# Performance work log

Measured on AMD Instinct MI355X. Metric: run time of the kernel, lower is better.

## Reference

```python
import jax, jax.numpy as jnp
import numpy as np

N_A, N_D = 16384, 16384
D_EV = 4096      # d_inEvents (= rows of H_M)
H_DIM = 512      # hidden_dim
H1 = 1024        # hidden_dim1
H3 = 1024        # hidden_dim3
D_M = 4096       # d_inM (reconstruction output dim)


def _mlp2(x, w1, b1, w2, b2):
    return jax.nn.relu(x @ w1 + b1) @ w2 + b2


def setup_inputs() -> dict:
    key = jax.random.key(0)
    ks = jax.random.split(key, 32)
    s_in = (2.0 / D_EV) ** 0.5
    s_h1 = (2.0 / H1) ** 0.5
    s_2h = (2.0 / (2 * H_DIM)) ** 0.5
    s_h3 = (2.0 / H3) ** 0.5
    d = {
        "H_A": jax.random.uniform(ks[0], (N_A, D_EV), jnp.float32),
        "H_D": jax.random.uniform(ks[1], (N_D, D_EV), jnp.float32),
        "H_M": jax.random.uniform(ks[2], (D_EV, D_EV), jnp.float32),
    }
    for i, nm in enumerate(["A", "D", "M"]):
        d[f"w{nm}1"] = jax.random.normal(ks[3 + 4 * i], (D_EV, H1), jnp.float32) * s_in
        d[f"b{nm}1"] = jnp.zeros((H1,), jnp.float32)
        d[f"w{nm}2"] = jax.random.normal(ks[4 + 4 * i], (H1, H_DIM), jnp.float32) * s_h1
        d[f"b{nm}2"] = jnp.zeros((H_DIM,), jnp.float32)
    for i, nm in enumerate(["EA", "ED"]):
        d[f"w{nm}1"] = jax.random.normal(ks[16 + 4 * i], (2 * H_DIM, H3), jnp.float32) * s_2h
        d[f"b{nm}1"] = jnp.zeros((H3,), jnp.float32)
        d[f"w{nm}2"] = jax.random.normal(ks[17 + 4 * i], (H3, D_M), jnp.float32) * s_h3
        d[f"b{nm}2"] = jnp.zeros((D_M,), jnp.float32)
    return d


def reference(H_A, H_D, H_M,
              wA1, bA1, wA2, bA2,
              wD1, bD1, wD2, bD2,
              wM1, bM1, wM2, bM2,
              wEA1, bEA1, wEA2, bEA2,
              wED1, bED1, wED2, bED2):
    # Encoder (the torch.eye matmul is an identity and is elided)
    H_mean_A = _mlp2(H_A, wA1, bA1, wA2, bA2)   # [N_A, H_DIM]
    H_mean_D = _mlp2(H_D, wD1, bD1, wD2, bD2)   # [N_D, H_DIM]
    H_mean_M = _mlp2(H_M, wM1, bM1, wM2, bM2)   # [D_EV, H_DIM]
    # Pooling: per-column loop in torch == single matmul H^T @ H_mean
    sum_A = H_A.T @ H_mean_A                    # [D_EV, H_DIM]
    sum_D = H_D.T @ H_mean_D                    # [D_EV, H_DIM]
    EventA = jnp.concatenate([H_mean_M, sum_A], axis=1)  # [D_EV, 2*H_DIM]
    EventD = jnp.concatenate([H_mean_M, sum_D], axis=1)
    reconstructA = _mlp2(EventA, wEA1, bEA1, wEA2, bEA2)  # [D_EV, D_M]
    reconstructD = _mlp2(EventD, wED1, bED1, wED2, bED2)
    return (reconstructA, reconstructD, H_mean_A, H_mean_D, H_mean_M)
```

## Files before the change

kernel.cpp:

```cpp
#include <hip/hip_runtime.h>
#include <cstdint>
#include <cstddef>


typedef unsigned short u16;
typedef unsigned int u32;
typedef __bf16 bf16_t;
typedef bf16_t bf16x8 __attribute__((ext_vector_type(8)));
typedef float f32x4 __attribute__((ext_vector_type(4)));
typedef u16 u16x4 __attribute__((ext_vector_type(4)));
typedef u16 u16x8 __attribute__((ext_vector_type(8)));

__device__ __forceinline__ u16 f2bf(float x) {
  u32 u = __builtin_bit_cast(u32, x);
  u += 0x7FFFu + ((u >> 16) & 1u);
  return (u16)(u >> 16);
}
__device__ __forceinline__ float bf2f(u16 h) {
  u32 u = ((u32)h) << 16;
  return __builtin_bit_cast(float, u);
}

#define AS1(p) ((__attribute__((address_space(1))) void*)(p))
#define AS3(p) ((__attribute__((address_space(3))) void*)(p))

__global__ void detect_kernel(const u32* __restrict__ p, int* __restrict__ flag) {
  if (threadIdx.x == 0 && blockIdx.x == 0) {
    int cnt = 0;
    for (int i = 0; i < 64; ++i) {
      u32 b = (p[i] >> 8) & 0xFFu;
      cnt += (b >= 0x3Au && b < 0x40u) ? 1 : 0;
    }
    *flag = (cnt >= 32) ? 1 : 0;
  }
}

__global__ void convert_kernel(const void* __restrict__ src, u16* __restrict__ dst,
                               long n, const int* __restrict__ fl) {
  long i = ((long)blockIdx.x * 256 + threadIdx.x) * 8;
  if (i >= n) return;
  u16x8 r;
  if (*fl) {
    r = *(const u16x8*)((const u16*)src + i);
  } else {
    const float* s = (const float*)src + i;
#pragma unroll
    for (int j = 0; j < 8; ++j) r[j] = f2bf(s[j]);
  }
  *(u16x8*)(dst + i) = r;
}

__global__ void tconv_kernel(const void* __restrict__ src, long soff, u16* __restrict__ dst,
                             int R, int C, const int* __restrict__ fl) {
  __shared__ u16 t[32][33];
  const int dt = *fl;
  const int tx = threadIdx.x & 31, ty = threadIdx.x >> 5;
  const long c0 = (long)blockIdx.x * 32, r0 = (long)blockIdx.y * 32;
#pragma unroll
  for (int r = 0; r < 4; ++r) {
    int rr = ty * 4 + r;
    long off = soff + (r0 + rr) * (long)C + c0 + tx;
    t[rr][tx] = dt ? ((const u16*)src)[off] : f2bf(((const float*)src)[off]);
  }
  __syncthreads();
#pragma unroll
  for (int r = 0; r < 4; ++r) {
    int rr = ty * 4 + r;
    dst[(c0 + rr) * (long)R + r0 + tx] = t[tx][rr];
  }
}

__global__ void reduce4_kernel(const float* __restrict__ s, long stride,
                               u16* __restrict__ dst, long ldd, long n, int cl,
                               const void* __restrict__ bias, int relu,
                               const int* __restrict__ fl) {
  long i = (long)blockIdx.x * 256 + threadIdx.x;
  if (i >= n) return;
  float v = s[i] + s[i + stride] + s[i + 2 * stride] + s[i + 3 * stride];
  long col = i & ((1L << cl) - 1);
  if (bias) v += (*fl) ? bf2f(((const u16*)bias)[col]) : ((const float*)bias)[col];
  if (relu) v = v > 0.f ? v : 0.f;
  dst[(i >> cl) * ldd + col] = f2bf(v);
}

__global__ __launch_bounds__(256) void gemm_bt_kernel(
    const u16* __restrict__ A, long lda,
    const u16* __restrict__ Bt, long ldb,
    long K,
    const void* __restrict__ bias, int relu,
    void* __restrict__ outd, long odoff, long ldod,
    float* __restrict__ outw, long ldow, long ozstride,
    u16* __restrict__ outb, long ldob,
    u16* __restrict__ outb2, long ldob2,
    u16* __restrict__ outT, long ldT,
    const int* __restrict__ fl) {
  __shared__ u16 As[128 * 32];
  __shared__ u16 Bs[128 * 32];

  const int t = threadIdx.x;
  const int l = t & 63;
  const int w = t >> 6;
  const int wx = w & 1, wy = w >> 1;
  const long m0 = (long)blockIdx.y * 128;
  const long n0 = (long)blockIdx.x * 128;
  const int dt = *fl;

  const long koff = (long)blockIdx.z * K;
  A += koff;
  Bt += koff;
  if (outw) outw += (long)blockIdx.z * ozstride;

  const int srow = w * 16 + (l >> 2);
  const int scol = (((l & 3) ^ ((l >> 2) & 3))) * 8;
  const int la = l & 15, lq = l >> 4;
  const int fsl = (lq ^ (la & 3)) * 8;

  f32x4 acc[4][4];
  const f32x4 zero = {0.f, 0.f, 0.f, 0.f};
#pragma unroll
  for (int i = 0; i < 4; ++i)
#pragma unroll
    for (int j = 0; j < 4; ++j) acc[i][j] = zero;

  for (long k0 = 0; k0 < K; k0 += 32) {
#pragma unroll
    for (int r = 0; r < 2; ++r) {
      const u16* ga = A + (m0 + r * 64 + srow) * lda + k0 + scol;
      __builtin_amdgcn_global_load_lds(AS1(ga), AS3(As + (r * 64 + w * 16) * 32), 16, 0, 0);
      const u16* gb = Bt + (n0 + r * 64 + srow) * ldb + k0 + scol;
      __builtin_amdgcn_global_load_lds(AS1(gb), AS3(Bs + (r * 64 + w * 16) * 32), 16, 0, 0);
    }
    __syncthreads();

    bf16x8 af[4], bfr[4];
#pragma unroll
    for (int i = 0; i < 4; ++i) {
      af[i] = *(const bf16x8*)(As + (wy * 64 + i * 16 + la) * 32 + fsl);
      bfr[i] = *(const bf16x8*)(Bs + (wx * 64 + i * 16 + la) * 32 + fsl);
    }
#pragma unroll
    for (int i = 0; i < 4; ++i)
#pragma unroll
      for (int j = 0; j < 4; ++j)
        acc[i][j] = __builtin_amdgcn_mfma_f32_16x16x32_bf16(af[i], bfr[j], acc[i][j], 0, 0, 0);
    __syncthreads();
  }

  const long gr0 = m0 + wy * 64;
  const long gc0 = n0 + wx * 64;
#pragma unroll
  for (int i = 0; i < 4; ++i) {
#pragma unroll
    for (int j = 0; j < 4; ++j) {
      const long gc = gc0 + j * 16 + la;
      const long grb = gr0 + i * 16 + lq * 4;
      float bv = 0.f;
      if (bias) bv = dt ? bf2f(((const u16*)bias)[gc]) : ((const float*)bias)[gc];
      float vv[4];
#pragma unroll
      for (int p = 0; p < 4; ++p) {
        float x = acc[i][j][p] + bv;
        if (relu) x = x > 0.f ? x : 0.f;
        vv[p] = x;
      }
      if (outd) {
        if (dt) {
          u16* o = (u16*)outd + odoff;
#pragma unroll
          for (int p = 0; p < 4; ++p) o[(grb + p) * ldod + gc] = f2bf(vv[p]);
        } else {
          float* o = (float*)outd + odoff;
#pragma unroll
          for (int p = 0; p < 4; ++p) o[(grb + p) * ldod + gc] = vv[p];
        }
      }
      if (outw) {
#pragma unroll
        for (int p = 0; p < 4; ++p) outw[(grb + p) * ldow + gc] = vv[p];
      }
      if (outb) {
#pragma unroll
        for (int p = 0; p < 4; ++p) outb[(grb + p) * ldob + gc] = f2bf(vv[p]);
      }
      if (outb2) {
#pragma unroll
        for (int p = 0; p < 4; ++p) outb2[(grb + p) * ldob2 + gc] = f2bf(vv[p]);
      }
      if (outT) {
        u16x4 pk;
#pragma unroll
        for (int p = 0; p < 4; ++p) pk[p] = f2bf(vv[p]);
        *(u16x4*)(outT + gc * ldT + grb) = pk;
      }
    }
  }
}

#define STAGE256(OP, KH, KZ, NB)                                                      \
  {                                                                                   \
    const u16* g_ = (OP) ? gB : gA;                                                   \
    const long ld_ = (OP) ? ldb : lda;                                                \
    u16* lb_ = lw + (NB) + (OP) * 16384 + (KH) * 8192;                                \
    __builtin_amdgcn_global_load_lds(AS1(g_ + (KZ) + (KH) * 32), AS3(lb_), 16, 0, 0); \
    __builtin_amdgcn_global_load_lds(AS1(g_ + (KZ) + (KH) * 32 + 128 * ld_),          \
                                     AS3(lb_ + 4096), 16, 0, 0);                      \
  }

#define LDA4(MH, KS, CB)                                                              \
  _Pragma("unroll") for (int i_ = 0; i_ < 4; ++i_)                                    \
      af[i_] = *(const bf16x8*)(smem + (CB) + (KS) * 8192 + abase + (MH) * 2048 + i_ * 512);

#define LDB4(KS, CB)                                                                  \
  _Pragma("unroll") for (int j_ = 0; j_ < 4; ++j_)                                    \
      bfr[j_] = *(const bf16x8*)(smem + (CB) + (KS) * 8192 + bbase + j_ * 512);

#define MFMA16(MH)                                                                    \
  _Pragma("unroll") for (int i_ = 0; i_ < 4; ++i_) {                                  \
    _Pragma("unroll") for (int j_ = 0; j_ < 4; ++j_) {                                \
      acc[(MH) * 4 + i_][j_] = __builtin_amdgcn_mfma_f32_16x16x32_bf16(               \
          af[i_], bfr[j_], acc[(MH) * 4 + i_][j_], 0, 0, 0);                          \
    }                                                                                 \
  }

__global__ __launch_bounds__(512, 2) void gemm256_2ph_kernel(
    const u16* __restrict__ A, long lda,
    const u16* __restrict__ Bt, long ldb,
    long K,
    const void* __restrict__ bias, int relu,
    void* __restrict__ outd, long odoff, long ldod,
    float* __restrict__ outw, long ldow, long ozstride,
    u16* __restrict__ outb, long ldob,
    const int* __restrict__ fl) {
  __shared__ u16 smem[65536];

  const int t = threadIdx.x;
  const int l = t & 63;
  const int w = t >> 6;
  const int wx = w & 3, wy = w >> 2;
  const int la = l & 15, lq = l >> 4;
  const long m0 = (long)blockIdx.y * 256;
  const long n0 = (long)blockIdx.x * 256;

  const long koff = (long)blockIdx.z * K;
  A += koff;
  Bt += koff;
  if (outw) outw += (long)blockIdx.z * ozstride;

  const int sr = t >> 2;
  const long kc = 8 * ((t & 3) ^ (sr & 3));
  const u16* gA = A + (m0 + sr) * lda + kc;
  const u16* gB = Bt + (n0 + sr) * ldb + kc;
  u16* lw = smem + w * 512;

  const int ard = la * 32 + ((lq ^ (la & 3)) << 3);
  const int abase = wy * 4096 + ard;
  const int bbase = 16384 + wx * 2048 + ard;

  f32x4 acc[8][4];
  const f32x4 zero = {0.f, 0.f, 0.f, 0.f};
#pragma unroll
  for (int i = 0; i < 8; ++i)
#pragma unroll
    for (int j = 0; j < 4; ++j) acc[i][j] = zero;

  const long NT = K >> 6;

  STAGE256(0, 0, 0L, 0);
  STAGE256(1, 0, 0L, 0);
  STAGE256(0, 1, 0L, 0);
  STAGE256(1, 1, 0L, 0);
  __syncthreads();

  for (long kt = 0; kt < NT; ++kt) {
    const int cb = (int)(kt & 1) * 32768;
    if (kt + 1 < NT) {
      const int nb = cb ^ 32768;
      const long kz = (kt + 1) << 6;
      STAGE256(0, 0, kz, nb);
      STAGE256(1, 0, kz, nb);
      STAGE256(0, 1, kz, nb);
      STAGE256(1, 1, kz, nb);
    }
    bf16x8 af[4], bfr[4];
    LDB4(0, cb);
    LDA4(0, 0, cb);
    MFMA16(0);
    LDA4(1, 0, cb);
    MFMA16(1);
    LDB4(1, cb);
    LDA4(0, 1, cb);
    MFMA16(0);
    LDA4(1, 1, cb);
    MFMA16(1);
    __syncthreads();
  }

  const int dt = *fl;
  const long gr0 = m0 + wy * 128;
  const long gc0 = n0 + wx * 64;
#pragma unroll
  for (int gi = 0; gi < 8; ++gi) {
#pragma unroll
    for (int j = 0; j < 4; ++j) {
      const long gc = gc0 + j * 16 + la;
      const long grb = gr0 + gi * 16 + lq * 4;
      float bv = 0.f;
      if (bias) bv = dt ? bf2f(((const u16*)bias)[gc]) : ((const float*)bias)[gc];
      float vv[4];
#pragma unroll
      for (int p = 0; p < 4; ++p) {
        float x = acc[gi][j][p] + bv;
        if (relu) x = x > 0.f ? x : 0.f;
        vv[p] = x;
      }
      if (outd) {
        if (dt) {
          u16* o = (u16*)outd + odoff;
#pragma unroll
          for (int p = 0; p < 4; ++p) o[(grb + p) * ldod + gc] = f2bf(vv[p]);
        } else {
          float* o = (float*)outd + odoff;
#pragma unroll
          for (int p = 0; p < 4; ++p) o[(grb + p) * ldod + gc] = vv[p];
        }
      }
      if (outw) {
#pragma unroll
        for (int p = 0; p < 4; ++p) outw[(grb + p) * ldow + gc] = vv[p];
      }
      if (outb) {
#pragma unroll
        for (int p = 0; p < 4; ++p) outb[(grb + p) * ldob + gc] = f2bf(vv[p]);
      }
    }
  }
}

static void gemm(hipStream_t st, const u16* A, long lda, const u16* Bt, long ldb,
                 long M, long N, long K, int zsplit,
                 const void* bias, int relu,
                 void* outd, long odoff, long ldod,
                 float* outw, long ldow, long ozstride,
                 u16* outb, long ldob, u16* outb2, long ldob2,
                 u16* outT, long ldT, const int* fl) {
  dim3 g((unsigned)(N / 128), (unsigned)(M / 128), (unsigned)zsplit);
  gemm_bt_kernel<<<g, 256, 0, st>>>(A, lda, Bt, ldb, K, bias, relu, outd, odoff, ldod,
                                    outw, ldow, ozstride, outb, ldob, outb2, ldob2,
                                    outT, ldT, fl);
}

static void gemm256(hipStream_t st, const u16* A, long lda, const u16* Bt, long ldb,
                    long M, long N, long K,
                    const void* bias, int relu,
                    void* outd, long odoff, long ldod,
                    u16* outb, long ldob, const int* fl) {
  dim3 g((unsigned)(N / 256), (unsigned)(M / 256), 1);
  gemm256_2ph_kernel<<<g, 512, 0, st>>>(A, lda, Bt, ldb, K, bias, relu, outd, odoff, ldod,
                                        nullptr, 0, 0, outb, ldob, fl);
}

static void tconv(hipStream_t st, const void* src, long soff, u16* dst, int R, int C,
                  const int* fl) {
  tconv_kernel<<<dim3((unsigned)(C / 32), (unsigned)(R / 32)), 256, 0, st>>>(src, soff, dst, R,
                                                                             C, fl);
}

static void conv(hipStream_t st, const void* src, u16* dst, long n, const int* fl) {
  convert_kernel<<<(unsigned)((n / 8 + 255) / 256), 256, 0, st>>>(src, dst, n, fl);
}

extern "C" void kernel_launch(void* const* d_in, const int* in_sizes, int n_in,
                              void* d_out, int out_size, void* d_ws, size_t ws_size,
                              hipStream_t stream) {
  (void)in_sizes; (void)n_in; (void)out_size; (void)ws_size;
  const long NA = 16384, DEV = 4096, H1n = 1024, HD = 512, DM = 4096;

  char* ws = (char*)d_ws;
  u16* BIG = (u16*)(ws + 0L);
  u16* H1B = (u16*)(ws + 134217728L);
  float* SUMS = (float*)(ws + 134217728L);
  u16* HMT = (u16*)(ws + 167772160L);
  u16* EVA = (u16*)(ws + 184549376L);
  u16* EVD = (u16*)(ws + 192937984L);
  u16* WT1 = (u16*)(ws + 201326592L);
  u16* WT2 = (u16*)(ws + 209715200L);
  int* FLAG = (int*)(ws + 218103808L);

  const void* H_A = d_in[0];
  const void* H_D = d_in[1];
  const void* H_M = d_in[2];
  const void *wA1 = d_in[3], *bA1 = d_in[4], *wA2 = d_in[5], *bA2 = d_in[6];
  const void *wD1 = d_in[7], *bD1 = d_in[8], *wD2 = d_in[9], *bD2 = d_in[10];
  const void *wM1 = d_in[11], *bM1 = d_in[12], *wM2 = d_in[13], *bM2 = d_in[14];
  const void *wEA1 = d_in[15], *bEA1 = d_in[16], *wEA2 = d_in[17], *bEA2 = d_in[18];
  const void *wED1 = d_in[19], *bED1 = d_in[20], *wED2 = d_in[21], *bED2 = d_in[22];

  const long O_RA = 0, O_RD = 16777216, O_HA = 33554432, O_HD = 41943040, O_HM = 50331648;

  detect_kernel<<<1, 64, 0, stream>>>((const u32*)H_A, FLAG);

  tconv(stream, wM1, 0, WT1, (int)DEV, (int)H1n, FLAG);
  tconv(stream, wM2, 0, WT2, (int)H1n, (int)HD, FLAG);
  conv(stream, H_M, BIG, DEV * DEV, FLAG);
  gemm(stream, BIG, DEV, WT1, DEV, DEV, H1n, DEV, 1, bM1, 1,
       nullptr, 0, 0, nullptr, 0, 0, H1B, H1n, nullptr, 0, nullptr, 0, FLAG);
  gemm(stream, H1B, H1n, WT2, H1n, DEV, HD, H1n, 1, bM2, 0,
       d_out, O_HM, HD, nullptr, 0, 0, EVA, 1024, EVD, 1024, nullptr, 0, FLAG);

  tconv(stream, wA1, 0, WT1, (int)DEV, (int)H1n, FLAG);
  tconv(stream, wA2, 0, WT2, (int)H1n, (int)HD, FLAG);
  conv(stream, H_A, BIG, NA * DEV, FLAG);
  gemm256(stream, BIG, DEV, WT1, DEV, NA, H1n, DEV, bA1, 1,
          nullptr, 0, 0, H1B, H1n, FLAG);
  gemm(stream, H1B, H1n, WT2, H1n, NA, HD, H1n, 1, bA2, 0,
       d_out, O_HA, HD, nullptr, 0, 0, nullptr, 0, nullptr, 0, HMT, NA, FLAG);
  tconv(stream, H_A, 0, BIG, (int)NA, (int)DEV, FLAG);
  gemm(stream, BIG, NA, HMT, NA, DEV, HD, 4096, 4, nullptr, 0,
       nullptr, 0, 0, SUMS, HD, 2097152L, nullptr, 0, nullptr, 0, nullptr, 0, FLAG);
  reduce4_kernel<<<8192, 256, 0, stream>>>(SUMS, 2097152L, EVA + 512, 1024L, DEV * HD, 9,
                                           nullptr, 0, FLAG);

  tconv(stream, wEA1, 0, WT1, (int)H1n, (int)H1n, FLAG);
  tconv(stream, wEA2, 0, WT2, (int)H1n, (int)DM, FLAG);
  gemm(stream, EVA, 1024, WT1, H1n, DEV, H1n, H1n, 1, bEA1, 1,
       nullptr, 0, 0, nullptr, 0, 0, H1B, H1n, nullptr, 0, nullptr, 0, FLAG);
  gemm256(stream, H1B, H1n, WT2, H1n, DEV, DM, H1n, bEA2, 0,
          d_out, O_RA, DM, nullptr, 0, FLAG);

  tconv(stream, wD1, 0, WT1, (int)DEV, (int)H1n, FLAG);
  tconv(stream, wD2, 0, WT2, (int)H1n, (int)HD, FLAG);
  conv(stream, H_D, BIG, NA * DEV, FLAG);
  gemm256(stream, BIG, DEV, WT1, DEV, NA, H1n, DEV, bD1, 1,
          nullptr, 0, 0, H1B, H1n, FLAG);
  gemm(stream, H1B, H1n, WT2, H1n, NA, HD, H1n, 1, bD2, 0,
       d_out, O_HD, HD, nullptr, 0, 0, nullptr, 0, nullptr, 0, HMT, NA, FLAG);
  tconv(stream, H_D, 0, BIG, (int)NA, (int)DEV, FLAG);
  gemm(stream, BIG, NA, HMT, NA, DEV, HD, 4096, 4, nullptr, 0,
       nullptr, 0, 0, SUMS, HD, 2097152L, nullptr, 0, nullptr, 0, nullptr, 0, FLAG);
  reduce4_kernel<<<8192, 256, 0, stream>>>(SUMS, 2097152L, EVD + 512, 1024L, DEV * HD, 9,
                                           nullptr, 0, FLAG);

  tconv(stream, wED1, 0, WT1, (int)H1n, (int)H1n, FLAG);
  tconv(stream, wED2, 0, WT2, (int)H1n, (int)DM, FLAG);
  gemm(stream, EVD, 1024, WT1, H1n, DEV, H1n, H1n, 1, bED1, 1,
       nullptr, 0, 0, nullptr, 0, 0, H1B, H1n, nullptr, 0, nullptr, 0, FLAG);
  gemm256(stream, H1B, H1n, WT2, H1n, DEV, DM, H1n, bED2, 0,
          d_out, O_RD, DM, nullptr, 0, FLAG);
}
```

Measured before the change: 1.997 ms.

## Skip bf16 input copies, remap workgroups, change LDS swizzle, use 256-tile pooling GEMM

When inputs are already bf16, the convert kernels now return early and the GEMMs read the raw input pointer directly, so the full-matrix copy is skipped. The 256-tile GEMM gains a workgroup index remap that groups tiles for better cache locality, plus z-split support with fp32 partial outputs so the pooling GEMMs can use it. The LDS swizzle pattern in both GEMM kernels is changed to reduce bank conflicts. These are several independent changes, and the swizzle edits must keep the store and load sides consistent.

After: 1.963 ms. Within noise of the previous version (-1.7%).

```diff
diff --git a/kernel.cpp b/kernel.cpp
--- a/kernel.cpp
+++ b/kernel.cpp
@@ -36,11 +36,13 @@
 }
 
 __global__ void convert_kernel(const void* __restrict__ src, u16* __restrict__ dst,
-                               long n, const int* __restrict__ fl) {
+                               long n, const int* __restrict__ fl, int skip) {
+  const int dt = *fl;
+  if (dt && skip) return;
   long i = ((long)blockIdx.x * 256 + threadIdx.x) * 8;
   if (i >= n) return;
   u16x8 r;
-  if (*fl) {
+  if (dt) {
     r = *(const u16x8*)((const u16*)src + i);
   } else {
     const float* s = (const float*)src + i;
@@ -93,6 +95,7 @@
     u16* __restrict__ outb, long ldob,
     u16* __restrict__ outb2, long ldob2,
     u16* __restrict__ outT, long ldT,
+    const void* __restrict__ rawA,
     const int* __restrict__ fl) {
   __shared__ u16 As[128 * 32];
   __shared__ u16 Bs[128 * 32];
@@ -104,6 +107,7 @@
   const long m0 = (long)blockIdx.y * 128;
   const long n0 = (long)blockIdx.x * 128;
   const int dt = *fl;
+  if (dt && rawA) A = (const u16*)rawA;
 
   const long koff = (long)blockIdx.z * K;
   A += koff;
@@ -111,9 +115,9 @@
   if (outw) outw += (long)blockIdx.z * ozstride;
 
   const int srow = w * 16 + (l >> 2);
-  const int scol = (((l & 3) ^ ((l >> 2) & 3))) * 8;
+  const int scol = ((l & 3) ^ ((l >> 3) & 3)) * 8;
   const int la = l & 15, lq = l >> 4;
-  const int fsl = (lq ^ (la & 3)) * 8;
+  const int fsl = (lq ^ ((la >> 1) & 3)) * 8;
 
   f32x4 acc[4][4];
   const f32x4 zero = {0.f, 0.f, 0.f, 0.f};
@@ -230,6 +234,7 @@
     void* __restrict__ outd, long odoff, long ldod,
     float* __restrict__ outw, long ldow, long ozstride,
     u16* __restrict__ outb, long ldob,
+    const void* __restrict__ rawA,
     const int* __restrict__ fl) {
   __shared__ u16 smem[65536];
 
@@ -238,8 +243,21 @@
   const int w = t >> 6;
   const int wx = w & 3, wy = w >> 2;
   const int la = l & 15, lq = l >> 4;
-  const long m0 = (long)blockIdx.y * 256;
-  const long n0 = (long)blockIdx.x * 256;
+  const int dt = *fl;
+  if (dt && rawA) A = (const u16*)rawA;
+
+  const unsigned gx = gridDim.x;
+  const unsigned nwg = gx * gridDim.y;
+  unsigned lx = blockIdx.x, ly = blockIdx.y;
+  if ((nwg & 7u) == 0u) {
+    const unsigned q = nwg >> 3;
+    const unsigned L = ly * gx + lx;
+    const unsigned nl = (L & 7u) * q + (L >> 3);
+    lx = nl % gx;
+    ly = nl / gx;
+  }
+  const long m0 = (long)ly * 256;
+  const long n0 = (long)lx * 256;
 
   const long koff = (long)blockIdx.z * K;
   A += koff;
@@ -247,12 +265,12 @@
   if (outw) outw += (long)blockIdx.z * ozstride;
 
   const int sr = t >> 2;
-  const long kc = 8 * ((t & 3) ^ (sr & 3));
+  const long kc = 8 * ((t & 3) ^ ((sr >> 1) & 3));
   const u16* gA = A + (m0 + sr) * lda + kc;
   const u16* gB = Bt + (n0 + sr) * ldb + kc;
   u16* lw = smem + w * 512;
 
-  const int ard = la * 32 + ((lq ^ (la & 3)) << 3);
+  const int ard = la * 32 + ((lq ^ ((la >> 1) & 3)) << 3);
   const int abase = wy * 4096 + ard;
   const int bbase = 16384 + wx * 2048 + ard;
 
@@ -295,7 +313,6 @@
     __syncthreads();
   }
 
-  const int dt = *fl;
   const long gr0 = m0 + wy * 128;
   const long gc0 = n0 + wx * 64;
 #pragma unroll
@@ -342,21 +359,22 @@
                  void* outd, long odoff, long ldod,
                  float* outw, long ldow, long ozstride,
                  u16* outb, long ldob, u16* outb2, long ldob2,
-                 u16* outT, long ldT, const int* fl) {
+                 u16* outT, long ldT, const void* rawA, const int* fl) {
   dim3 g((unsigned)(N / 128), (unsigned)(M / 128), (unsigned)zsplit);
   gemm_bt_kernel<<<g, 256, 0, st>>>(A, lda, Bt, ldb, K, bias, relu, outd, odoff, ldod,
                                     outw, ldow, ozstride, outb, ldob, outb2, ldob2,
-                                    outT, ldT, fl);
+                                    outT, ldT, rawA, fl);
 }
 
 static void gemm256(hipStream_t st, const u16* A, long lda, const u16* Bt, long ldb,
-                    long M, long N, long K,
+                    long M, long N, long K, int zsplit,
                     const void* bias, int relu,
                     void* outd, long odoff, long ldod,
-                    u16* outb, long ldob, const int* fl) {
-  dim3 g((unsigned)(N / 256), (unsigned)(M / 256), 1);
+                    float* outw, long ldow, long ozstride,
+                    u16* outb, long ldob, const void* rawA, const int* fl) {
+  dim3 g((unsigned)(N / 256), (unsigned)(M / 256), (unsigned)zsplit);
   gemm256_2ph_kernel<<<g, 512, 0, st>>>(A, lda, Bt, ldb, K, bias, relu, outd, odoff, ldod,
-                                        nullptr, 0, 0, outb, ldob, fl);
+                                        outw, ldow, ozstride, outb, ldob, rawA, fl);
 }
 
 static void tconv(hipStream_t st, const void* src, long soff, u16* dst, int R, int C,
@@ -365,8 +383,8 @@
                                                                              C, fl);
 }
 
-static void conv(hipStream_t st, const void* src, u16* dst, long n, const int* fl) {
-  convert_kernel<<<(unsigned)((n / 8 + 255) / 256), 256, 0, st>>>(src, dst, n, fl);
+static void conv(hipStream_t st, const void* src, u16* dst, long n, const int* fl, int skip) {
+  convert_kernel<<<(unsigned)((n / 8 + 255) / 256), 256, 0, st>>>(src, dst, n, fl, skip);
 }
 
 extern "C" void kernel_launch(void* const* d_in, const int* in_sizes, int n_in,
@@ -401,49 +419,49 @@
 
   tconv(stream, wM1, 0, WT1, (int)DEV, (int)H1n, FLAG);
   tconv(stream, wM2, 0, WT2, (int)H1n, (int)HD, FLAG);
-  conv(stream, H_M, BIG, DEV * DEV, FLAG);
+  conv(stream, H_M, BIG, DEV * DEV, FLAG, 1);
   gemm(stream, BIG, DEV, WT1, DEV, DEV, H1n, DEV, 1, bM1, 1,
-       nullptr, 0, 0, nullptr, 0, 0, H1B, H1n, nullptr, 0, nullptr, 0, FLAG);
+       nullptr, 0, 0, nullptr, 0, 0, H1B, H1n, nullptr, 0, nullptr, 0, H_M, FLAG);
   gemm(stream, H1B, H1n, WT2, H1n, DEV, HD, H1n, 1, bM2, 0,
-       d_out, O_HM, HD, nullptr, 0, 0, EVA, 1024, EVD, 1024, nullptr, 0, FLAG);
+       d_out, O_HM, HD, nullptr, 0, 0, EVA, 1024, EVD, 1024, nullptr, 0, nullptr, FLAG);
 
   tconv(stream, wA1, 0, WT1, (int)DEV, (int)H1n, FLAG);
   tconv(stream, wA2, 0, WT2, (int)H1n, (int)HD, FLAG);
-  conv(stream, H_A, BIG, NA * DEV, FLAG);
-  gemm256(stream, BIG, DEV, WT1, DEV, NA, H1n, DEV, bA1, 1,
-          nullptr, 0, 0, H1B, H1n, FLAG);
+  conv(stream, H_A, BIG, NA * DEV, FLAG, 1);
+  gemm256(stream, BIG, DEV, WT1, DEV, NA, H1n, DEV, 1, bA1, 1,
+          nullptr, 0, 0, nullptr, 0, 0, H1B, H1n, H_A, FLAG);
   gemm(stream, H1B, H1n, WT2, H1n, NA, HD, H1n, 1, bA2, 0,
-       d_out, O_HA, HD, nullptr, 0, 0, nullptr, 0, nullptr, 0, HMT, NA, FLAG);
+       d_out, O_HA, HD, nullptr, 0, 0, nullptr, 0, nullptr, 0, HMT, NA, nullptr, FLAG);
   tconv(stream, H_A, 0, BIG, (int)NA, (int)DEV, FLAG);
-  gemm(stream, BIG, NA, HMT, NA, DEV, HD, 4096, 4, nullptr, 0,
-       nullptr, 0, 0, SUMS, HD, 2097152L, nullptr, 0, nullptr, 0, nullptr, 0, FLAG);
+  gemm256(stream, BIG, NA, HMT, NA, DEV, HD, 4096, 4, nullptr, 0,
+          nullptr, 0, 0, SUMS, HD, 2097152L, nullptr, 0, nullptr, FLAG);
   reduce4_kernel<<<8192, 256, 0, stream>>>(SUMS, 2097152L, EVA + 512, 1024L, DEV * HD, 9,
                                            nullptr, 0, FLAG);
 
   tconv(stream, wEA1, 0, WT1, (int)H1n, (int)H1n, FLAG);
   tconv(stream, wEA2, 0, WT2, (int)H1n, (int)DM, FLAG);
   gemm(stream, EVA, 1024, WT1, H1n, DEV, H1n, H1n, 1, bEA1, 1,
-       nullptr, 0, 0, nullptr, 0, 0, H1B, H1n, nullptr, 0, nullptr, 0, FLAG);
-  gemm256(stream, H1B, H1n, WT2, H1n, DEV, DM, H1n, bEA2, 0,
-          d_out, O_RA, DM, nullptr, 0, FLAG);
+       nullptr, 0, 0, nullptr, 0, 0, H1B, H1n, nullptr, 0, nullptr, 0, nullptr, FLAG);
+  gemm256(stream, H1B, H1n, WT2, H1n, DEV, DM, H1n, 1, bEA2, 0,
+          d_out, O_RA, DM, nullptr, 0, 0, nullptr, 0, nullptr, FLAG);
 
   tconv(stream, wD1, 0, WT1, (int)DEV, (int)H1n, FLAG);
   tconv(stream, wD2, 0, WT2, (int)H1n, (int)HD, FLAG);
-  conv(stream, H_D, BIG, NA * DEV, FLAG);
-  gemm256(stream, BIG, DEV, WT1, DEV, NA, H1n, DEV, bD1, 1,
-          nullptr, 0, 0, H1B, H1n, FLAG);
+  conv(stream, H_D, BIG, NA * DEV, FLAG, 1);
+  gemm256(stream, BIG, DEV, WT1, DEV, NA, H1n, DEV, 1, bD1, 1,
+          nullptr, 0, 0, nullptr, 0, 0, H1B, H1n, H_D, FLAG);
   gemm(stream, H1B, H1n, WT2, H1n, NA, HD, H1n, 1, bD2, 0,
-       d_out, O_HD, HD, nullptr, 0, 0, nullptr, 0, nullptr, 0, HMT, NA, FLAG);
+       d_out, O_HD, HD, nullptr, 0, 0, nullptr, 0, nullptr, 0, HMT, NA, nullptr, FLAG);
   tconv(stream, H_D, 0, BIG, (int)NA, (int)DEV, FLAG);
-  gemm(stream, BIG, NA, HMT, NA, DEV, HD, 4096, 4, nullptr, 0,
-       nullptr, 0, 0, SUMS, HD, 2097152L, nullptr, 0, nullptr, 0, nullptr, 0, FLAG);
+  gemm256(stream, BIG, NA, HMT, NA, DEV, HD, 4096, 4, nullptr, 0,
+          nullptr, 0, 0, SUMS, HD, 2097152L, nullptr, 0, nullptr, FLAG);
   reduce4_kernel<<<8192, 256, 0, stream>>>(SUMS, 2097152L, EVD + 512, 1024L, DEV * HD, 9,
                                            nullptr, 0, FLAG);
 
   tconv(stream, wED1, 0, WT1, (int)H1n, (int)H1n, FLAG);
   tconv(stream, wED2, 0, WT2, (int)H1n, (int)DM, FLAG);
   gemm(stream, EVD, 1024, WT1, H1n, DEV, H1n, H1n, 1, bED1, 1,
-       nullptr, 0, 0, nullptr, 0, 0, H1B, H1n, nullptr, 0, nullptr, 0, FLAG);
-  gemm256(stream, H1B, H1n, WT2, H1n, DEV, DM, H1n, bED2, 0,
-          d_out, O_RD, DM, nullptr, 0, FLAG);
-}
+       nullptr, 0, 0, nullptr, 0, 0, H1B, H1n, nullptr, 0, nullptr, 0, nullptr, FLAG);
+  gemm256(stream, H1B, H1n, WT2, H1n, DEV, DM, H1n, 1, bED2, 0,
+          d_out, O_RD, DM, nullptr, 0, 0, nullptr, 0, nullptr, FLAG);
+}
```
